# Kernel optimization log

Measured on AMD Instinct MI355X. Metric: run time of the kernel, lower is better.

The kernel has to match this reference:

```python
import jax, jax.numpy as jnp
import numpy as np

D = 1024; H = 16; DH = 64; L = 24; S = 4096; DFF = 4096
QB = 7; NC = 2 ** QB; TOPK = 10; EOS = NC + 1
SCALE = float(1.0 / np.sqrt(DH))


def _ln(x, g):
    m = jnp.mean(x, axis=-1, keepdims=True)
    v = jnp.var(x, axis=-1, keepdims=True)
    return (x - m) * jax.lax.rsqrt(v + 1e-5) * g


def _mlp(h, w1, b1, w2, b2, w3, b3):
    h = jax.nn.relu(h @ w1 + b1)
    h = jax.nn.relu(h @ w2 + b2)
    return h @ w3 + b3


def _decode(x, k_cache, v_cache, ln1_g, Wq, Wk, Wv, Wo, ln2_g, Wg, Wu, Wd, lnf_g):
    # single-token decode through L pre-norm layers with KV cache
    def step(h, xs):
        l1, wq, wk, wv, wo, l2, wg, wu, wd, K, V = xs
        hn = _ln(h, l1)
        q = (hn @ wq).reshape(H, DH)
        kn = (hn @ wk).reshape(1, H, DH)
        vn = (hn @ wv).reshape(1, H, DH)
        Kf = jnp.concatenate([K, kn], axis=0)  # [S+1,H,DH]
        Vf = jnp.concatenate([V, vn], axis=0)
        att = jax.nn.softmax(jnp.einsum('hd,shd->hs', q, Kf) * SCALE, axis=-1)
        o = jnp.einsum('hs,shd->hd', att, Vf).reshape(D)
        h = h + o @ wo
        hn = _ln(h, l2)
        h = h + (jax.nn.gelu(hn @ wg) * (hn @ wu)) @ wd  # GLU FF
        return h, None

    res, _ = jax.lax.scan(step, x, (ln1_g, Wq, Wk, Wv, Wo, ln2_g, Wg, Wu, Wd, k_cache, v_cache))
    return _ln(res, lnf_g)


def setup_inputs() -> dict:
    key = jax.random.key(0)
    ks = jax.random.split(key, 40)
    def r(i, shape, s=0.02):
        return jax.random.normal(ks[i], shape, dtype=jnp.float32) * s
    inp = {
        'x': r(0, (D,), 1.0),
        'k_cache': r(1, (L, S, H, DH), 1.0),
        'v_cache': r(2, (L, S, H, DH), 1.0),
        'ln1_g': jnp.ones((L, D), jnp.float32),
        'Wq': r(3, (L, D, D)), 'Wk': r(4, (L, D, D)), 'Wv': r(5, (L, D, D)), 'Wo': r(6, (L, D, D)),
        'ln2_g': jnp.ones((L, D), jnp.float32),
        'Wg': r(7, (L, D, DFF)), 'Wu': r(8, (L, D, DFF)), 'Wd': r(9, (L, DFF, D)),
        'lnf_g': jnp.ones((D,), jnp.float32),
        'h1_w1': r(10, (D, D)), 'h1_b1': jnp.zeros((D,), jnp.float32),
        'h1_w2': r(11, (D, D)), 'h1_b2': jnp.zeros((D,), jnp.float32),
        'h1_w3': r(12, (D, NC + 2)), 'h1_b3': jnp.zeros((NC + 2,), jnp.float32),
        'h2_w1': r(13, (2 * D, D)), 'h2_b1': jnp.zeros((D,), jnp.float32),
        'h2_w2': r(14, (D, D)), 'h2_b2': jnp.zeros((D,), jnp.float32),
        'h2_w3': r(15, (D, NC)), 'h2_b3': jnp.zeros((NC,), jnp.float32),
        'h3_w1': r(16, (3 * D, D)), 'h3_b1': jnp.zeros((D,), jnp.float32),
        'h3_w2': r(17, (D, D)), 'h3_b2': jnp.zeros((D,), jnp.float32),
        'h3_w3': r(18, (D, NC)), 'h3_b3': jnp.zeros((NC,), jnp.float32),
        'c1_emb': r(19, (NC, D), 1.0),
        'c2_emb': r(20, (NC, D), 1.0),
    }
    return inp


def reference(x, k_cache, v_cache, ln1_g, Wq, Wk, Wv, Wo, ln2_g, Wg, Wu, Wd, lnf_g,
              h1_w1, h1_b1, h1_w2, h1_b2, h1_w3, h1_b3,
              h2_w1, h2_b1, h2_w2, h2_b2, h2_w3, h2_b3,
              h3_w1, h3_b1, h3_w2, h3_b2, h3_w3, h3_b3,
              c1_emb, c2_emb):
    res = _decode(x, k_cache, v_cache, ln1_g, Wq, Wk, Wv, Wo, ln2_g, Wg, Wu, Wd, lnf_g)

    k1, k2, k3 = jax.random.split(jax.random.key(42), 3)

    # stage 1: z coordinate (quantized) with EOS-masked top-k sampling
    logits_z = _mlp(res, h1_w1, h1_b1, h1_w2, h1_b2, h1_w3, h1_b3)  # [NC+2]
    tpz, tiz = jax.lax.top_k(jax.nn.softmax(logits_z), TOPK)
    is_eos = tiz[0] == EOS
    mp = tpz * (tiz != EOS).astype(tpz.dtype)
    mp = mp / mp.sum()
    z = jnp.where(is_eos, EOS, tiz[jax.random.categorical(k1, jnp.log(mp + 1e-9))])
    emb_z = c1_emb[jnp.minimum(z, NC - 1)]

    # stage 2: y coordinate
    logits_y = _mlp(jnp.concatenate([res, emb_z]), h2_w1, h2_b1, h2_w2, h2_b2, h2_w3, h2_b3)
    tpy, tiy = jax.lax.top_k(jax.nn.softmax(logits_y), TOPK)
    y = tiy[jax.random.categorical(k2, jnp.log(tpy + 1e-9))]
    emb_y = c2_emb[y]

    # stage 3: x coordinate
    logits_x = _mlp(jnp.concatenate([res, emb_z, emb_y]), h3_w1, h3_b1, h3_w2, h3_b2, h3_w3, h3_b3)
    tpx, tix = jax.lax.top_k(jax.nn.softmax(logits_x), TOPK)
    xc = tix[jax.random.categorical(k3, jnp.log(tpx + 1e-9))]

    xyz = jnp.stack([xc, y, z])
    logits_cat = jnp.concatenate([logits_z, logits_y, logits_x])  # [130+128+128]=386
    return xyz, logits_cat
```

## Files before the change

kernel.cpp:

```cpp
#include <hip/hip_runtime.h>
#include <cstdint>
#include <cstring>
#include <cmath>

constexpr int kH    = 16;
constexpr int kL    = 24;
constexpr int kS    = 4096;
constexpr int kEOS  = 129;
constexpr float kSCALE = 0.125f;
constexpr int kNS   = 32;
constexpr int kTOK  = kS / kNS;

struct G10 { float g[10]; };


__device__ __forceinline__ float wave_sum(float v) {
  v += __shfl_xor(v, 32, 64); v += __shfl_xor(v, 16, 64);
  v += __shfl_xor(v, 8, 64);  v += __shfl_xor(v, 4, 64);
  v += __shfl_xor(v, 2, 64);  v += __shfl_xor(v, 1, 64);
  return v;
}
__device__ __forceinline__ float wave_max(float v) {
  v = fmaxf(v, __shfl_xor(v, 32, 64)); v = fmaxf(v, __shfl_xor(v, 16, 64));
  v = fmaxf(v, __shfl_xor(v, 8, 64));  v = fmaxf(v, __shfl_xor(v, 4, 64));
  v = fmaxf(v, __shfl_xor(v, 2, 64));  v = fmaxf(v, __shfl_xor(v, 1, 64));
  return v;
}
__device__ __forceinline__ float block_sum4(float v, float* red) {
  v = wave_sum(v);
  if ((threadIdx.x & 63) == 0) red[threadIdx.x >> 6] = v;
  __syncthreads();
  float s = red[0] + red[1] + red[2] + red[3];
  __syncthreads();
  return s;
}
__device__ __forceinline__ float block_max4(float v, float* red) {
  v = wave_max(v);
  if ((threadIdx.x & 63) == 0) red[threadIdx.x >> 6] = v;
  __syncthreads();
  float s = fmaxf(fmaxf(red[0], red[1]), fmaxf(red[2], red[3]));
  __syncthreads();
  return s;
}

__device__ __forceinline__ void ln_stats(const float* __restrict__ h, float* red,
                                         float& mean, float& rs) {
  int tid = threadIdx.x;
  float v0 = h[tid], v1 = h[tid + 256], v2 = h[tid + 512], v3 = h[tid + 768];
  float s = block_sum4(v0 + v1 + v2 + v3, red);
  mean = s * (1.0f / 1024.0f);
  float d0 = v0 - mean, d1 = v1 - mean, d2 = v2 - mean, d3 = v3 - mean;
  float sq = block_sum4(d0 * d0 + d1 * d1 + d2 * d2 + d3 * d3, red);
  rs = 1.0f / sqrtf(sq * (1.0f / 1024.0f) + 1e-5f);
}

__device__ __forceinline__ float gelu_f(float x) {
  float t = tanhf(0.7978845608028654f * (x + 0.044715f * x * x * x));
  return 0.5f * x * (1.0f + t);
}


__global__ __launch_bounds__(256) void k_ln_qkv(const float* __restrict__ h,
                                                const float* __restrict__ g,
                                                const float* __restrict__ Wq,
                                                const float* __restrict__ Wk,
                                                const float* __restrict__ Wv,
                                                float* __restrict__ qkv_part,
                                                float* __restrict__ hres) {
  __shared__ float red4[4];
  __shared__ float xs[64];
  __shared__ float4 sh4[256];
  int tid = threadIdx.x;
  float mean, rs;
  ln_stats(h, red4, mean, rs);
  int by = blockIdx.y, rb = by * 64;
  if (tid < 64) xs[tid] = (h[rb + tid] - mean) * rs * g[rb + tid];
  if (blockIdx.x == 0 && tid < 64) hres[rb + tid] = h[rb + tid];
  __syncthreads();
  int c4 = tid & 63, w = tid >> 6;
  int vcol4 = blockIdx.x * 64 + c4;
  int mat = vcol4 >> 8;
  const float* W = (mat == 0) ? Wq : ((mat == 1) ? Wk : Wv);
  const float4* W4 = reinterpret_cast<const float4*>(W);
  int wcol4 = vcol4 & 255;
  float4 acc = {0.f, 0.f, 0.f, 0.f};
  int r0 = w * 16;
  #pragma unroll
  for (int i = 0; i < 16; ++i) {
    int j = r0 + i;
    float xv = xs[j];
    float4 wv = W4[(size_t)(rb + j) * 256 + wcol4];
    acc.x += xv * wv.x; acc.y += xv * wv.y; acc.z += xv * wv.z; acc.w += xv * wv.w;
  }
  sh4[tid] = acc;
  __syncthreads();
  if (tid < 64) {
    float4 a = sh4[tid], b = sh4[tid + 64], c = sh4[tid + 128], d = sh4[tid + 192];
    a.x += b.x + c.x + d.x; a.y += b.y + c.y + d.y;
    a.z += b.z + c.z + d.z; a.w += b.w + c.w + d.w;
    reinterpret_cast<float4*>(qkv_part)[(size_t)by * 768 + blockIdx.x * 64 + tid] = a;
  }
}

__global__ __launch_bounds__(256) void k_attn(const float* __restrict__ qkv_part,
                                              const float* __restrict__ Kc,
                                              const float* __restrict__ Vc,
                                              float* __restrict__ part) {
  __shared__ float4 q4[16];
  __shared__ float4 kn4[16];
  __shared__ float4 vn4[16];
  __shared__ float sc[132];
  __shared__ float red4[4];
  __shared__ float4 ored[16][17];
  int split = blockIdx.x, head = blockIdx.y;
  int tid = threadIdx.x;
  if (tid < 64) {
    float s = 0.f;
    #pragma unroll
    for (int p = 0; p < 16; ++p) s += qkv_part[p * 3072 + head * 64 + tid];
    ((float*)q4)[tid] = s;
  } else if (tid < 128) {
    int d = tid - 64; float s = 0.f;
    #pragma unroll
    for (int p = 0; p < 16; ++p) s += qkv_part[p * 3072 + 1024 + head * 64 + d];
    ((float*)kn4)[d] = s;
  } else if (tid < 192) {
    int d = tid - 128; float s = 0.f;
    #pragma unroll
    for (int p = 0; p < 16; ++p) s += qkv_part[p * 3072 + 2048 + head * 64 + d];
    ((float*)vn4)[d] = s;
  }
  __syncthreads();
  int base = split * kTOK;
  int count = kTOK + (split == kNS - 1 ? 1 : 0);
  int wv = tid >> 6, lane = tid & 63, grp = lane >> 4, l16 = lane & 15;
  float4 qf = q4[l16];
  for (int t = wv * 4 + grp; t < count; t += 16) {
    float4 kf = (t < kTOK)
      ? reinterpret_cast<const float4*>(Kc + (size_t)(base + t) * 1024 + head * 64)[l16]
      : kn4[l16];
    float d = qf.x * kf.x + qf.y * kf.y + qf.z * kf.z + qf.w * kf.w;
    d += __shfl_xor(d, 1, 16); d += __shfl_xor(d, 2, 16);
    d += __shfl_xor(d, 4, 16); d += __shfl_xor(d, 8, 16);
    if (l16 == 0) sc[t] = d * kSCALE;
  }
  __syncthreads();
  float v = (tid < count) ? sc[tid] : -1e30f;
  float m = block_max4(v, red4);
  float pexp = 0.f;
  if (tid < count) { pexp = expf(sc[tid] - m); sc[tid] = pexp; }
  float l = block_sum4(pexp, red4);
  float4 acc = {0.f, 0.f, 0.f, 0.f};
  for (int t = wv * 4 + grp; t < count; t += 16) {
    float4 vf = (t < kTOK)
      ? reinterpret_cast<const float4*>(Vc + (size_t)(base + t) * 1024 + head * 64)[l16]
      : vn4[l16];
    float p = sc[t];
    acc.x += p * vf.x; acc.y += p * vf.y; acc.z += p * vf.z; acc.w += p * vf.w;
  }
  ored[wv * 4 + grp][l16] = acc;
  __syncthreads();
  float* pp = &part[(size_t)(head * kNS + split) * 68];
  if (tid < 16) {
    float4 s = ored[0][tid];
    #pragma unroll
    for (int k = 1; k < 16; ++k) {
      float4 b = ored[k][tid];
      s.x += b.x; s.y += b.y; s.z += b.z; s.w += b.w;
    }
    reinterpret_cast<float4*>(pp + 4)[tid] = s;
  }
  if (tid == 0) { pp[0] = m; pp[1] = l; }
}

__global__ __launch_bounds__(256) void k_comb_wo(const float* __restrict__ part,
                                                 const float* __restrict__ Wo,
                                                 float* __restrict__ hout) {
  __shared__ float o[64];
  __shared__ float4 sh4[256];
  int tid = threadIdx.x;
  int head = blockIdx.y;
  if (tid < 64) {
    const float* pp = part + (size_t)(head * kNS) * 68;
    float m = -1e30f;
    for (int s = 0; s < kNS; ++s) m = fmaxf(m, pp[s * 68]);
    float l = 0.f, acc = 0.f;
    for (int s = 0; s < kNS; ++s) {
      float e = expf(pp[s * 68] - m);
      l += e * pp[s * 68 + 1];
      acc += e * pp[s * 68 + 4 + tid];
    }
    o[tid] = acc / l;
  }
  __syncthreads();
  int c4 = tid & 63, w = tid >> 6;
  int vcol4 = blockIdx.x * 64 + c4;
  const float4* W4 = reinterpret_cast<const float4*>(Wo);
  float4 acc = {0.f, 0.f, 0.f, 0.f};
  int r0 = w * 16;
  #pragma unroll
  for (int i = 0; i < 16; ++i) {
    int r = r0 + i;
    float xv = o[r];
    float4 wv = W4[(size_t)(head * 64 + r) * 256 + vcol4];
    acc.x += xv * wv.x; acc.y += xv * wv.y; acc.z += xv * wv.z; acc.w += xv * wv.w;
  }
  sh4[tid] = acc;
  __syncthreads();
  if (tid < 64) {
    float4 a = sh4[tid], b = sh4[tid + 64], c = sh4[tid + 128], d = sh4[tid + 192];
    a.x += b.x + c.x + d.x; a.y += b.y + c.y + d.y;
    a.z += b.z + c.z + d.z; a.w += b.w + c.w + d.w;
    int vcol = (blockIdx.x * 64 + tid) * 4;
    atomicAdd(&hout[vcol],     a.x);
    atomicAdd(&hout[vcol + 1], a.y);
    atomicAdd(&hout[vcol + 2], a.z);
    atomicAdd(&hout[vcol + 3], a.w);
  }
}

__global__ __launch_bounds__(256) void k_ln_gu(const float* __restrict__ h,
                                               const float* __restrict__ g,
                                               const float* __restrict__ Wg,
                                               const float* __restrict__ Wu,
                                               float* __restrict__ gu_part,
                                               float* __restrict__ hres) {
  __shared__ float red4[4];
  __shared__ float xs[64];
  __shared__ float4 sh4[256];
  int tid = threadIdx.x;
  float mean, rs;
  ln_stats(h, red4, mean, rs);
  int by = blockIdx.y, rb = by * 64;
  if (tid < 64) xs[tid] = (h[rb + tid] - mean) * rs * g[rb + tid];
  if (blockIdx.x == 0 && tid < 64) hres[rb + tid] = h[rb + tid];
  __syncthreads();
  int c4 = tid & 63, w = tid >> 6;
  int vcol4 = blockIdx.x * 64 + c4;
  int mat = vcol4 >> 10;
  const float4* W4 = reinterpret_cast<const float4*>(mat ? Wu : Wg);
  int wcol4 = vcol4 & 1023;
  float4 acc = {0.f, 0.f, 0.f, 0.f};
  int r0 = w * 16;
  #pragma unroll
  for (int i = 0; i < 16; ++i) {
    int j = r0 + i;
    float xv = xs[j];
    float4 wv = W4[(size_t)(rb + j) * 1024 + wcol4];
    acc.x += xv * wv.x; acc.y += xv * wv.y; acc.z += xv * wv.z; acc.w += xv * wv.w;
  }
  sh4[tid] = acc;
  __syncthreads();
  if (tid < 64) {
    float4 a = sh4[tid], b = sh4[tid + 64], c = sh4[tid + 128], d = sh4[tid + 192];
    a.x += b.x + c.x + d.x; a.y += b.y + c.y + d.y;
    a.z += b.z + c.z + d.z; a.w += b.w + c.w + d.w;
    reinterpret_cast<float4*>(gu_part)[(size_t)by * 2048 + blockIdx.x * 64 + tid] = a;
  }
}

__global__ __launch_bounds__(256) void k_act_wd(const float* __restrict__ gu_part,
                                                const float* __restrict__ Wd,
                                                float* __restrict__ hout) {
  __shared__ float xs[64];
  __shared__ float4 sh4[256];
  int tid = threadIdx.x;
  int by = blockIdx.y, rb = by * 64;
  if (tid < 64) {
    float gs = 0.f, us = 0.f;
    #pragma unroll
    for (int p = 0; p < 16; ++p) {
      gs += gu_part[p * 8192 + rb + tid];
      us += gu_part[p * 8192 + 4096 + rb + tid];
    }
    xs[tid] = gelu_f(gs) * us;
  }
  __syncthreads();
  int c4 = tid & 63, w = tid >> 6;
  int vcol4 = blockIdx.x * 64 + c4;
  const float4* W4 = reinterpret_cast<const float4*>(Wd);
  float4 acc = {0.f, 0.f, 0.f, 0.f};
  int r0 = w * 16;
  #pragma unroll
  for (int i = 0; i < 16; ++i) {
    int j = r0 + i;
    float xv = xs[j];
    float4 wv = W4[(size_t)(rb + j) * 256 + vcol4];
    acc.x += xv * wv.x; acc.y += xv * wv.y; acc.z += xv * wv.z; acc.w += xv * wv.w;
  }
  sh4[tid] = acc;
  __syncthreads();
  if (tid < 64) {
    float4 a = sh4[tid], b = sh4[tid + 64], c = sh4[tid + 128], d = sh4[tid + 192];
    a.x += b.x + c.x + d.x; a.y += b.y + c.y + d.y;
    a.z += b.z + c.z + d.z; a.w += b.w + c.w + d.w;
    int vcol = (blockIdx.x * 64 + tid) * 4;
    atomicAdd(&hout[vcol],     a.x);
    atomicAdd(&hout[vcol + 1], a.y);
    atomicAdd(&hout[vcol + 2], a.z);
    atomicAdd(&hout[vcol + 3], a.w);
  }
}


__global__ __launch_bounds__(256) void k_head_g1(const float* __restrict__ hA,
                                                 const float* __restrict__ lnfg,
                                                 const float* __restrict__ catE,
                                                 const float* __restrict__ W,
                                                 float* __restrict__ t1_part,
                                                 const float* __restrict__ b3,
                                                 float* __restrict__ logits, int n3) {
  __shared__ float red4[4];
  __shared__ float xs[64];
  __shared__ float4 sh4[256];
  int tid = threadIdx.x;
  float mean, rs;
  ln_stats(hA, red4, mean, rs);
  int by = blockIdx.y, rb = by * 64;
  if (blockIdx.x == 0 && by == 0 && tid < n3) logits[tid] = b3[tid];
  if (tid < 64) {
    int r = rb + tid;
    xs[tid] = (r < 1024) ? (hA[r] - mean) * rs * lnfg[r] : catE[r - 1024];
  }
  __syncthreads();
  int c4 = tid & 63, w = tid >> 6;
  int vcol4 = blockIdx.x * 64 + c4;
  const float4* W4 = reinterpret_cast<const float4*>(W);
  float4 acc = {0.f, 0.f, 0.f, 0.f};
  int r0 = w * 16;
  #pragma unroll
  for (int i = 0; i < 16; ++i) {
    float xv = xs[r0 + i];
    float4 wv = W4[(size_t)(rb + r0 + i) * 256 + vcol4];
    acc.x += xv * wv.x; acc.y += xv * wv.y; acc.z += xv * wv.z; acc.w += xv * wv.w;
  }
  sh4[tid] = acc;
  __syncthreads();
  if (tid < 64) {
    float4 a = sh4[tid], b = sh4[tid + 64], c = sh4[tid + 128], d = sh4[tid + 192];
    a.x += b.x + c.x + d.x; a.y += b.y + c.y + d.y;
    a.z += b.z + c.z + d.z; a.w += b.w + c.w + d.w;
    reinterpret_cast<float4*>(t1_part)[(size_t)by * 256 + blockIdx.x * 64 + tid] = a;
  }
}

__global__ __launch_bounds__(256) void k_head_g2(const float* __restrict__ t1_part,
                                                 int ny,
                                                 const float* __restrict__ b1,
                                                 const float* __restrict__ W,
                                                 float* __restrict__ t2_part) {
  __shared__ float xs[64];
  __shared__ float4 sh4[256];
  int tid = threadIdx.x;
  int by = blockIdx.y, rb = by * 64;
  if (tid < 64) {
    float s = b1[rb + tid];
    for (int p = 0; p < ny; ++p) s += t1_part[p * 1024 + rb + tid];
    xs[tid] = fmaxf(s, 0.f);
  }
  __syncthreads();
  int c4 = tid & 63, w = tid >> 6;
  int vcol4 = blockIdx.x * 64 + c4;
  const float4* W4 = reinterpret_cast<const float4*>(W);
  float4 acc = {0.f, 0.f, 0.f, 0.f};
  int r0 = w * 16;
  #pragma unroll
  for (int i = 0; i < 16; ++i) {
    int j = r0 + i;
    float xv = xs[j];
    float4 wv = W4[(size_t)(rb + j) * 256 + vcol4];
    acc.x += xv * wv.x; acc.y += xv * wv.y; acc.z += xv * wv.z; acc.w += xv * wv.w;
  }
  sh4[tid] = acc;
  __syncthreads();
  if (tid < 64) {
    float4 a = sh4[tid], b = sh4[tid + 64], c = sh4[tid + 128], d = sh4[tid + 192];
    a.x += b.x + c.x + d.x; a.y += b.y + c.y + d.y;
    a.z += b.z + c.z + d.z; a.w += b.w + c.w + d.w;
    reinterpret_cast<float4*>(t2_part)[(size_t)by * 256 + blockIdx.x * 64 + tid] = a;
  }
}

__global__ __launch_bounds__(256) void k_head_g3(const float* __restrict__ t2_part,
                                                 const float* __restrict__ b2,
                                                 const float* __restrict__ W,
                                                 float* __restrict__ logits, int n3) {
  __shared__ float xs[64];
  int tid = threadIdx.x;
  int rb = blockIdx.x * 64;
  if (tid < 64) {
    float s = b2[rb + tid];
    #pragma unroll
    for (int p = 0; p < 16; ++p) s += t2_part[p * 1024 + rb + tid];
    xs[tid] = fmaxf(s, 0.f);
  }
  __syncthreads();
  if (tid < n3) {
    float acc = 0.f;
    for (int i = 0; i < 64; ++i) acc += xs[i] * W[(size_t)(rb + i) * n3 + tid];
    atomicAdd(&logits[tid], acc);
  }
}


__global__ void k_sample1(const float* __restrict__ logits,
                          const float* __restrict__ c1_emb,
                          float* __restrict__ embdst,
                          float* __restrict__ out_xyz,
                          G10 gb) {
  __shared__ int zsh;
  int tid = threadIdx.x;
  if (tid == 0) {
    float p[130];
    float mx = -1e30f;
    for (int i = 0; i < 130; ++i) mx = fmaxf(mx, logits[i]);
    float s = 0.f;
    for (int i = 0; i < 130; ++i) { p[i] = expf(logits[i] - mx); s += p[i]; }
    for (int i = 0; i < 130; ++i) p[i] /= s;
    float tp[10]; int ti[10];
    for (int k = 0; k < 10; ++k) {
      float best = -1.f; int bi = 0;
      for (int i = 0; i < 130; ++i)
        if (p[i] > best) { best = p[i]; bi = i; }
      tp[k] = best; ti[k] = bi; p[bi] = -2.f;
    }
    int is_eos = (ti[0] == kEOS);
    float mp[10]; float ssum = 0.f;
    for (int k = 0; k < 10; ++k) {
      mp[k] = tp[k] * ((ti[k] != kEOS) ? 1.f : 0.f);
      ssum += mp[k];
    }
    float bestsc = -1e30f; int ba = 0;
    for (int k = 0; k < 10; ++k) {
      float sc = logf(mp[k] / ssum + 1e-9f) + gb.g[k];
      if (sc > bestsc) { bestsc = sc; ba = k; }
    }
    int z = is_eos ? kEOS : ti[ba];
    zsh = z;
    out_xyz[2] = (float)z;
  }
  __syncthreads();
  int zi = zsh; if (zi > 127) zi = 127;
  for (int i = tid; i < 1024; i += blockDim.x)
    embdst[i] = c1_emb[(size_t)zi * 1024 + i];
}

__global__ void k_sample23(const float* __restrict__ logits,
                           const float* __restrict__ emb,
                           float* __restrict__ embdst,
                           float* __restrict__ outslot,
                           G10 gb) {
  __shared__ int ysh;
  int tid = threadIdx.x;
  if (tid == 0) {
    float p[128];
    float mx = -1e30f;
    for (int i = 0; i < 128; ++i) mx = fmaxf(mx, logits[i]);
    float s = 0.f;
    for (int i = 0; i < 128; ++i) { p[i] = expf(logits[i] - mx); s += p[i]; }
    for (int i = 0; i < 128; ++i) p[i] /= s;
    float tp[10]; int ti[10];
    for (int k = 0; k < 10; ++k) {
      float best = -1.f; int bi = 0;
      for (int i = 0; i < 128; ++i)
        if (p[i] > best) { best = p[i]; bi = i; }
      tp[k] = best; ti[k] = bi; p[bi] = -2.f;
    }
    float bestsc = -1e30f; int ba = 0;
    for (int k = 0; k < 10; ++k) {
      float sc = logf(tp[k] + 1e-9f) + gb.g[k];
      if (sc > bestsc) { bestsc = sc; ba = k; }
    }
    int y = ti[ba];
    ysh = y;
    *outslot = (float)y;
  }
  __syncthreads();
  if (emb != nullptr) {
    int y = ysh;
    for (int i = tid; i < 1024; i += blockDim.x)
      embdst[i] = emb[(size_t)y * 1024 + i];
  }
}


static inline uint32_t rotl32(uint32_t x, uint32_t r) { return (x << r) | (x >> (32 - r)); }

static void threefry2x32(uint32_t k0, uint32_t k1, uint32_t x0, uint32_t x1,
                         uint32_t* o0, uint32_t* o1) {
  uint32_t ks0 = k0, ks1 = k1, ks2 = k0 ^ k1 ^ 0x1BD11BDAu;
  const uint32_t R0[4] = {13, 15, 26, 6};
  const uint32_t R1[4] = {17, 29, 16, 24};
  x0 += ks0; x1 += ks1;
  for (int j = 0; j < 4; ++j) { x0 += x1; x1 = rotl32(x1, R0[j]); x1 ^= x0; }
  x0 += ks1; x1 += ks2 + 1u;
  for (int j = 0; j < 4; ++j) { x0 += x1; x1 = rotl32(x1, R1[j]); x1 ^= x0; }
  x0 += ks2; x1 += ks0 + 2u;
  for (int j = 0; j < 4; ++j) { x0 += x1; x1 = rotl32(x1, R0[j]); x1 ^= x0; }
  x0 += ks0; x1 += ks1 + 3u;
  for (int j = 0; j < 4; ++j) { x0 += x1; x1 = rotl32(x1, R1[j]); x1 ^= x0; }
  x0 += ks1; x1 += ks2 + 4u;
  for (int j = 0; j < 4; ++j) { x0 += x1; x1 = rotl32(x1, R0[j]); x1 ^= x0; }
  x0 += ks2; x1 += ks0 + 5u;
  *o0 = x0; *o1 = x1;
}

static void gumbel10_part(uint32_t k0, uint32_t k1, float* g) {
  const float tiny = 1.1754943508222875e-38f;
  for (int i = 0; i < 10; ++i) {
    uint32_t a, c;
    threefry2x32(k0, k1, 0u, (uint32_t)i, &a, &c);
    uint32_t bits = a ^ c;
    uint32_t fb = (bits >> 9) | 0x3f800000u;
    float f; memcpy(&f, &fb, 4);
    f -= 1.0f;
    float u = f * (1.0f - tiny) + tiny;
    if (u < tiny) u = tiny;
    g[i] = -logf(-logf(u));
  }
}


extern "C" void kernel_launch(void* const* d_in, const int* in_sizes, int n_in,
                              void* d_out, int out_size, void* d_ws, size_t ws_size,
                              hipStream_t stream) {
  (void)in_sizes; (void)n_in; (void)out_size; (void)ws_size;
  const float* x      = (const float*)d_in[0];
  const float* kcache = (const float*)d_in[1];
  const float* vcache = (const float*)d_in[2];
  const float* ln1g   = (const float*)d_in[3];
  const float* Wq     = (const float*)d_in[4];
  const float* Wk     = (const float*)d_in[5];
  const float* Wv     = (const float*)d_in[6];
  const float* Wo     = (const float*)d_in[7];
  const float* ln2g   = (const float*)d_in[8];
  const float* Wg     = (const float*)d_in[9];
  const float* Wu     = (const float*)d_in[10];
  const float* Wd     = (const float*)d_in[11];
  const float* lnfg   = (const float*)d_in[12];
  const float* h1w1 = (const float*)d_in[13]; const float* h1b1 = (const float*)d_in[14];
  const float* h1w2 = (const float*)d_in[15]; const float* h1b2 = (const float*)d_in[16];
  const float* h1w3 = (const float*)d_in[17]; const float* h1b3 = (const float*)d_in[18];
  const float* h2w1 = (const float*)d_in[19]; const float* h2b1 = (const float*)d_in[20];
  const float* h2w2 = (const float*)d_in[21]; const float* h2b2 = (const float*)d_in[22];
  const float* h2w3 = (const float*)d_in[23]; const float* h2b3 = (const float*)d_in[24];
  const float* h3w1 = (const float*)d_in[25]; const float* h3b1 = (const float*)d_in[26];
  const float* h3w2 = (const float*)d_in[27]; const float* h3b2 = (const float*)d_in[28];
  const float* h3w3 = (const float*)d_in[29]; const float* h3b3 = (const float*)d_in[30];
  const float* c1emb = (const float*)d_in[31];
  const float* c2emb = (const float*)d_in[32];

  float* ws = (float*)d_ws;
  float* hA   = ws;
  float* hB   = ws + 1024;
  float* qkvp = ws + 2048;
  float* part = ws + 51200;
  float* gup  = ws + 86016;
  float* catE = ws + 217088;
  float* t2p  = ws + 219136;
  float* t1p  = gup;
  float* out  = (float*)d_out;

  for (int l = 0; l < kL; ++l) {
    const float* Wq_l = Wq + (size_t)l * 1024 * 1024;
    const float* Wk_l = Wk + (size_t)l * 1024 * 1024;
    const float* Wv_l = Wv + (size_t)l * 1024 * 1024;
    const float* Wo_l = Wo + (size_t)l * 1024 * 1024;
    const float* Wg_l = Wg + (size_t)l * 1024 * 4096;
    const float* Wu_l = Wu + (size_t)l * 1024 * 4096;
    const float* Wd_l = Wd + (size_t)l * 4096 * 1024;
    const float* Kc_l = kcache + (size_t)l * kS * 1024;
    const float* Vc_l = vcache + (size_t)l * kS * 1024;
    const float* h_in = (l == 0) ? x : hA;

    k_ln_qkv<<<dim3(12, 16), 256, 0, stream>>>(h_in, ln1g + (size_t)l * 1024,
                                               Wq_l, Wk_l, Wv_l, qkvp, hB);
    k_attn<<<dim3(kNS, kH), 256, 0, stream>>>(qkvp, Kc_l, Vc_l, part);
    k_comb_wo<<<dim3(4, kH), 256, 0, stream>>>(part, Wo_l, hB);
    k_ln_gu<<<dim3(32, 16), 256, 0, stream>>>(hB, ln2g + (size_t)l * 1024,
                                              Wg_l, Wu_l, gup, hA);
    k_act_wd<<<dim3(4, 64), 256, 0, stream>>>(gup, Wd_l, hA);
  }

  uint32_t k1a, k1b, k2a, k2b, k3a, k3b;
  threefry2x32(0u, 42u, 0u, 0u, &k1a, &k1b);
  threefry2x32(0u, 42u, 0u, 1u, &k2a, &k2b);
  threefry2x32(0u, 42u, 0u, 2u, &k3a, &k3b);
  G10 G1, G2, G3;
  gumbel10_part(k1a, k1b, G1.g);
  gumbel10_part(k2a, k2b, G2.g);
  gumbel10_part(k3a, k3b, G3.g);

  k_head_g1<<<dim3(4, 16), 256, 0, stream>>>(hA, lnfg, catE, h1w1, t1p, h1b3, out + 3, 130);
  k_head_g2<<<dim3(4, 16), 256, 0, stream>>>(t1p, 16, h1b1, h1w2, t2p);
  k_head_g3<<<16, 256, 0, stream>>>(t2p, h1b2, h1w3, out + 3, 130);
  k_sample1<<<1, 256, 0, stream>>>(out + 3, c1emb, catE, out, G1);

  k_head_g1<<<dim3(4, 32), 256, 0, stream>>>(hA, lnfg, catE, h2w1, t1p, h2b3, out + 133, 128);
  k_head_g2<<<dim3(4, 16), 256, 0, stream>>>(t1p, 32, h2b1, h2w2, t2p);
  k_head_g3<<<16, 256, 0, stream>>>(t2p, h2b2, h2w3, out + 133, 128);
  k_sample23<<<1, 256, 0, stream>>>(out + 133, c2emb, catE + 1024, out + 1, G2);

  k_head_g1<<<dim3(4, 48), 256, 0, stream>>>(hA, lnfg, catE, h3w1, t1p, h3b3, out + 261, 128);
  k_head_g2<<<dim3(4, 16), 256, 0, stream>>>(t1p, 48, h3b1, h3w2, t2p);
  k_head_g3<<<16, 256, 0, stream>>>(t2p, h3b2, h3w3, out + 261, 128);
  k_sample23<<<1, 256, 0, stream>>>(out + 261, nullptr, nullptr, out + 0, G3);
}
```

Before: 1.354 ms.

## Prefetch V into registers in attention and widen grids for Wo and head GEMVs

The attention split kernel now fully unrolls its 128-token K and V loops, handles the new token as a separate tail, and issues all V loads into registers before the softmax reductions so their latency overlaps the barrier and reductions. The Wo-combine and head MLP GEMV kernels are restructured so each block covers 16 float4 columns with 16 row groups instead of 64 columns with 4 groups, which quadruples the grid size to use more CUs on these small GEMVs. The cost is more register pressure in attention, a longer in-block reduction, and in k_comb_wo the per-head softmax combine is repeated across four times as many blocks.

```diff
diff --git a/kernel.cpp b/kernel.cpp
--- a/kernel.cpp
+++ b/kernel.cpp
@@ -132,17 +132,34 @@
   }
   __syncthreads();
   int base = split * kTOK;
-  int count = kTOK + (split == kNS - 1 ? 1 : 0);
+  bool last = (split == kNS - 1);
+  int count = kTOK + (last ? 1 : 0);
   int wv = tid >> 6, lane = tid & 63, grp = lane >> 4, l16 = lane & 15;
+  int g0 = wv * 4 + grp;
   float4 qf = q4[l16];
-  for (int t = wv * 4 + grp; t < count; t += 16) {
-    float4 kf = (t < kTOK)
-      ? reinterpret_cast<const float4*>(Kc + (size_t)(base + t) * 1024 + head * 64)[l16]
-      : kn4[l16];
+  const float4* K4 = reinterpret_cast<const float4*>(Kc);
+  const float4* V4 = reinterpret_cast<const float4*>(Vc);
+  #pragma unroll
+  for (int i = 0; i < 8; ++i) {
+    int t = g0 + 16 * i;
+    float4 kf = K4[(size_t)(base + t) * 256 + head * 16 + l16];
     float d = qf.x * kf.x + qf.y * kf.y + qf.z * kf.z + qf.w * kf.w;
     d += __shfl_xor(d, 1, 16); d += __shfl_xor(d, 2, 16);
     d += __shfl_xor(d, 4, 16); d += __shfl_xor(d, 8, 16);
     if (l16 == 0) sc[t] = d * kSCALE;
+  }
+  if (last && g0 == 0) {
+    float4 kf = kn4[l16];
+    float d = qf.x * kf.x + qf.y * kf.y + qf.z * kf.z + qf.w * kf.w;
+    d += __shfl_xor(d, 1, 16); d += __shfl_xor(d, 2, 16);
+    d += __shfl_xor(d, 4, 16); d += __shfl_xor(d, 8, 16);
+    if (l16 == 0) sc[128] = d * kSCALE;
+  }
+  float4 vreg[8];
+  #pragma unroll
+  for (int i = 0; i < 8; ++i) {
+    int t = g0 + 16 * i;
+    vreg[i] = V4[(size_t)(base + t) * 256 + head * 16 + l16];
   }
   __syncthreads();
   float v = (tid < count) ? sc[tid] : -1e30f;
@@ -151,14 +168,19 @@
   if (tid < count) { pexp = expf(sc[tid] - m); sc[tid] = pexp; }
   float l = block_sum4(pexp, red4);
   float4 acc = {0.f, 0.f, 0.f, 0.f};
-  for (int t = wv * 4 + grp; t < count; t += 16) {
-    float4 vf = (t < kTOK)
-      ? reinterpret_cast<const float4*>(Vc + (size_t)(base + t) * 1024 + head * 64)[l16]
-      : vn4[l16];
+  #pragma unroll
+  for (int i = 0; i < 8; ++i) {
+    int t = g0 + 16 * i;
     float p = sc[t];
+    acc.x += p * vreg[i].x; acc.y += p * vreg[i].y;
+    acc.z += p * vreg[i].z; acc.w += p * vreg[i].w;
+  }
+  if (last && g0 == 0) {
+    float p = sc[128];
+    float4 vf = vn4[l16];
     acc.x += p * vf.x; acc.y += p * vf.y; acc.z += p * vf.z; acc.w += p * vf.w;
   }
-  ored[wv * 4 + grp][l16] = acc;
+  ored[g0][l16] = acc;
   __syncthreads();
   float* pp = &part[(size_t)(head * kNS + split) * 68];
   if (tid < 16) {
@@ -179,7 +201,7 @@
   __shared__ float o[64];
   __shared__ float4 sh4[256];
   int tid = threadIdx.x;
-  int head = blockIdx.y;
+  int head = blockIdx.y, bx = blockIdx.x;
   if (tid < 64) {
     const float* pp = part + (size_t)(head * kNS) * 68;
     float m = -1e30f;
@@ -193,13 +215,13 @@
     o[tid] = acc / l;
   }
   __syncthreads();
-  int c4 = tid & 63, w = tid >> 6;
-  int vcol4 = blockIdx.x * 64 + c4;
+  int c4 = tid & 15, w = tid >> 4;
+  int vcol4 = bx * 16 + c4;
   const float4* W4 = reinterpret_cast<const float4*>(Wo);
   float4 acc = {0.f, 0.f, 0.f, 0.f};
-  int r0 = w * 16;
-  #pragma unroll
-  for (int i = 0; i < 16; ++i) {
+  int r0 = w * 4;
+  #pragma unroll
+  for (int i = 0; i < 4; ++i) {
     int r = r0 + i;
     float xv = o[r];
     float4 wv = W4[(size_t)(head * 64 + r) * 256 + vcol4];
@@ -207,11 +229,14 @@
   }
   sh4[tid] = acc;
   __syncthreads();
-  if (tid < 64) {
-    float4 a = sh4[tid], b = sh4[tid + 64], c = sh4[tid + 128], d = sh4[tid + 192];
-    a.x += b.x + c.x + d.x; a.y += b.y + c.y + d.y;
-    a.z += b.z + c.z + d.z; a.w += b.w + c.w + d.w;
-    int vcol = (blockIdx.x * 64 + tid) * 4;
+  if (tid < 16) {
+    float4 a = sh4[tid];
+    #pragma unroll
+    for (int k = 1; k < 16; ++k) {
+      float4 b = sh4[k * 16 + tid];
+      a.x += b.x; a.y += b.y; a.z += b.z; a.w += b.w;
+    }
+    int vcol = (bx * 16 + tid) * 4;
     atomicAdd(&hout[vcol],     a.x);
     atomicAdd(&hout[vcol + 1], a.y);
     atomicAdd(&hout[vcol + 2], a.z);
@@ -323,24 +348,27 @@
     xs[tid] = (r < 1024) ? (hA[r] - mean) * rs * lnfg[r] : catE[r - 1024];
   }
   __syncthreads();
-  int c4 = tid & 63, w = tid >> 6;
-  int vcol4 = blockIdx.x * 64 + c4;
+  int c4 = tid & 15, w = tid >> 4;
+  int vcol4 = blockIdx.x * 16 + c4;
   const float4* W4 = reinterpret_cast<const float4*>(W);
   float4 acc = {0.f, 0.f, 0.f, 0.f};
-  int r0 = w * 16;
-  #pragma unroll
-  for (int i = 0; i < 16; ++i) {
+  int r0 = w * 4;
+  #pragma unroll
+  for (int i = 0; i < 4; ++i) {
     float xv = xs[r0 + i];
     float4 wv = W4[(size_t)(rb + r0 + i) * 256 + vcol4];
     acc.x += xv * wv.x; acc.y += xv * wv.y; acc.z += xv * wv.z; acc.w += xv * wv.w;
   }
   sh4[tid] = acc;
   __syncthreads();
-  if (tid < 64) {
-    float4 a = sh4[tid], b = sh4[tid + 64], c = sh4[tid + 128], d = sh4[tid + 192];
-    a.x += b.x + c.x + d.x; a.y += b.y + c.y + d.y;
-    a.z += b.z + c.z + d.z; a.w += b.w + c.w + d.w;
-    reinterpret_cast<float4*>(t1_part)[(size_t)by * 256 + blockIdx.x * 64 + tid] = a;
+  if (tid < 16) {
+    float4 a = sh4[tid];
+    #pragma unroll
+    for (int k = 1; k < 16; ++k) {
+      float4 b = sh4[k * 16 + tid];
+      a.x += b.x; a.y += b.y; a.z += b.z; a.w += b.w;
+    }
+    reinterpret_cast<float4*>(t1_part)[(size_t)by * 256 + blockIdx.x * 16 + tid] = a;
   }
 }
 
@@ -359,25 +387,27 @@
     xs[tid] = fmaxf(s, 0.f);
   }
   __syncthreads();
-  int c4 = tid & 63, w = tid >> 6;
-  int vcol4 = blockIdx.x * 64 + c4;
+  int c4 = tid & 15, w = tid >> 4;
+  int vcol4 = blockIdx.x * 16 + c4;
   const float4* W4 = reinterpret_cast<const float4*>(W);
   float4 acc = {0.f, 0.f, 0.f, 0.f};
-  int r0 = w * 16;
-  #pragma unroll
-  for (int i = 0; i < 16; ++i) {
-    int j = r0 + i;
-    float xv = xs[j];
-    float4 wv = W4[(size_t)(rb + j) * 256 + vcol4];
+  int r0 = w * 4;
+  #pragma unroll
+  for (int i = 0; i < 4; ++i) {
+    float xv = xs[r0 + i];
+    float4 wv = W4[(size_t)(rb + r0 + i) * 256 + vcol4];
     acc.x += xv * wv.x; acc.y += xv * wv.y; acc.z += xv * wv.z; acc.w += xv * wv.w;
   }
   sh4[tid] = acc;
   __syncthreads();
-  if (tid < 64) {
-    float4 a = sh4[tid], b = sh4[tid + 64], c = sh4[tid + 128], d = sh4[tid + 192];
-    a.x += b.x + c.x + d.x; a.y += b.y + c.y + d.y;
-    a.z += b.z + c.z + d.z; a.w += b.w + c.w + d.w;
-    reinterpret_cast<float4*>(t2_part)[(size_t)by * 256 + blockIdx.x * 64 + tid] = a;
+  if (tid < 16) {
+    float4 a = sh4[tid];
+    #pragma unroll
+    for (int k = 1; k < 16; ++k) {
+      float4 b = sh4[k * 16 + tid];
+      a.x += b.x; a.y += b.y; a.z += b.z; a.w += b.w;
+    }
+    reinterpret_cast<float4*>(t2_part)[(size_t)by * 256 + blockIdx.x * 16 + tid] = a;
   }
 }
 
@@ -576,7 +606,7 @@
     k_ln_qkv<<<dim3(12, 16), 256, 0, stream>>>(h_in, ln1g + (size_t)l * 1024,
                                                Wq_l, Wk_l, Wv_l, qkvp, hB);
     k_attn<<<dim3(kNS, kH), 256, 0, stream>>>(qkvp, Kc_l, Vc_l, part);
-    k_comb_wo<<<dim3(4, kH), 256, 0, stream>>>(part, Wo_l, hB);
+    k_comb_wo<<<dim3(16, kH), 256, 0, stream>>>(part, Wo_l, hB);
     k_ln_gu<<<dim3(32, 16), 256, 0, stream>>>(hB, ln2g + (size_t)l * 1024,
                                               Wg_l, Wu_l, gup, hA);
     k_act_wd<<<dim3(4, 64), 256, 0, stream>>>(gup, Wd_l, hA);
@@ -591,18 +621,18 @@
   gumbel10_part(k2a, k2b, G2.g);
   gumbel10_part(k3a, k3b, G3.g);
 
-  k_head_g1<<<dim3(4, 16), 256, 0, stream>>>(hA, lnfg, catE, h1w1, t1p, h1b3, out + 3, 130);
-  k_head_g2<<<dim3(4, 16), 256, 0, stream>>>(t1p, 16, h1b1, h1w2, t2p);
+  k_head_g1<<<dim3(16, 16), 256, 0, stream>>>(hA, lnfg, catE, h1w1, t1p, h1b3, out + 3, 130);
+  k_head_g2<<<dim3(16, 16), 256, 0, stream>>>(t1p, 16, h1b1, h1w2, t2p);
   k_head_g3<<<16, 256, 0, stream>>>(t2p, h1b2, h1w3, out + 3, 130);
   k_sample1<<<1, 256, 0, stream>>>(out + 3, c1emb, catE, out, G1);
 
-  k_head_g1<<<dim3(4, 32), 256, 0, stream>>>(hA, lnfg, catE, h2w1, t1p, h2b3, out + 133, 128);
-  k_head_g2<<<dim3(4, 16), 256, 0, stream>>>(t1p, 32, h2b1, h2w2, t2p);
+  k_head_g1<<<dim3(16, 32), 256, 0, stream>>>(hA, lnfg, catE, h2w1, t1p, h2b3, out + 133, 128);
+  k_head_g2<<<dim3(16, 16), 256, 0, stream>>>(t1p, 32, h2b1, h2w2, t2p);
   k_head_g3<<<16, 256, 0, stream>>>(t2p, h2b2, h2w3, out + 133, 128);
   k_sample23<<<1, 256, 0, stream>>>(out + 133, c2emb, catE + 1024, out + 1, G2);
 
-  k_head_g1<<<dim3(4, 48), 256, 0, stream>>>(hA, lnfg, catE, h3w1, t1p, h3b3, out + 261, 128);
-  k_head_g2<<<dim3(4, 16), 256, 0, stream>>>(t1p, 48, h3b1, h3w2, t2p);
+  k_head_g1<<<dim3(16, 48), 256, 0, stream>>>(hA, lnfg, catE, h3w1, t1p, h3b3, out + 261, 128);
+  k_head_g2<<<dim3(16, 16), 256, 0, stream>>>(t1p, 48, h3b1, h3w2, t2p);
   k_head_g3<<<16, 256, 0, stream>>>(t2p, h3b2, h3w3, out + 261, 128);
   k_sample23<<<1, 256, 0, stream>>>(out + 261, nullptr, nullptr, out + 0, G3);
 }
```

Result: faster. 1.241 ms (-8.3%).
